# Kernel tuning notes

Measured on AMD Instinct MI355X. Metric: run time of the kernel, lower is better.

## Reference

```python
import jax, jax.numpy as jnp
import numpy as np

N, L, HID = 8192, 256, 128   # rows, input_len, hidden_size
H, NLIN = 2, 2               # n_heads, n_linear
EPS = 1e-5


def setup_inputs() -> dict:
    key = jax.random.key(0)
    ks = jax.random.split(key, 8)
    # attention params (torch.randn in source; scaled 0.02 for numerical sanity of softmax logits)
    Q = jax.random.normal(ks[0], (H, L, HID), jnp.float32) * 0.02
    K = jax.random.normal(ks[1], (H, L, HID), jnp.float32) * 0.02
    V_down = jax.random.normal(ks[2], (H, L, HID), jnp.float32) * 0.02
    V_up = jax.random.normal(ks[3], (H, HID, L), jnp.float32) * 0.02
    # nn.Linear(input_len, input_len): uniform(-1/sqrt(L), 1/sqrt(L))
    bnd = 1.0 / np.sqrt(L)
    W = jax.random.uniform(ks[4], (NLIN, L, L), jnp.float32, -bnd, bnd)
    b = jax.random.uniform(ks[5], (NLIN, L), jnp.float32, -bnd, bnd)
    x = jax.random.normal(ks[6], (N, L), jnp.float32)
    return {"x": x, "Q": Q, "K": K, "V_down": V_down, "V_up": V_up, "W": W, "b": b}


def _batch_norm(z):
    # custom BatchNorm1d: per-feature normalization over the batch (row) dim, no affine
    m = jnp.mean(z, axis=0, keepdims=True)
    v = jnp.var(z, axis=0, keepdims=True)
    return (z - m) * jax.lax.rsqrt(v + EPS)


def reference(x, Q, K, V_down, V_up, W, b):
    h = _batch_norm(x)                              # [N, L]
    dE = jnp.zeros_like(h)
    for i in range(Q.shape[0]):                     # small fixed head count
        q = h @ Q[i]                                # [N, HID]
        k = h @ K[i]                                # [N, HID]
        A = jax.nn.softmax(q @ k.T, axis=1)         # [N, N]
        dE = dE + A @ (h @ V_down[i]) @ V_up[i]     # low-rank value path
    h = _batch_norm(h + dE)
    for j in range(W.shape[0]):                     # per-row Linear+ReLU loop == batched matmul
        h = jax.nn.relu(h @ W[j].T + b[j])
    return h
```

## Files before the change

### kernel.cpp

```cpp
#include <hip/hip_runtime.h>
#include <hip/hip_bf16.h>

constexpr int Nrows = 8192;
constexpr int L     = 256;
constexpr int D     = 128;
constexpr float EPS = 1e-5f;

typedef __bf16 bf16x8 __attribute__((ext_vector_type(8)));
typedef __bf16 bf16x4 __attribute__((ext_vector_type(4)));
typedef float  f32x4  __attribute__((ext_vector_type(4)));

#define MFMA16(a, b, c) __builtin_amdgcn_mfma_f32_16x16x32_bf16((a), (b), (c), 0, 0, 0)

__global__ void k_cvt_params(const float* __restrict__ Q, const float* __restrict__ K,
                             const float* __restrict__ Vd, const float* __restrict__ Vup,
                             const float* __restrict__ W,
                             __bf16* __restrict__ Bt, __bf16* __restrict__ VupT,
                             __bf16* __restrict__ Wb) {
    int i = blockIdx.x * 256 + threadIdx.x;
    if (i < 6 * 128 * 256) {
        int g = i >> 15; int r = i & 32767; int d = r >> 8; int l = r & 255;
        const float* src = (g % 3 == 0 ? Q : (g % 3 == 1 ? K : Vd)) + (g / 3) * (L * D);
        Bt[i] = (__bf16)src[l * D + d];
    } else if (i < 8 * 128 * 256) {
        int j = i - 6 * 128 * 256;
        int h = j >> 15; int r = j & 32767; int l = r >> 7; int d = r & 127;
        VupT[j] = (__bf16)Vup[h * (D * L) + d * L + l];
    } else {
        int j = i - 8 * 128 * 256;
        Wb[j] = (__bf16)W[j];
    }
}

__global__ void k_bn_stats(const float* __restrict__ x, float* __restrict__ sum,
                           float* __restrict__ sq) {
    int col = threadIdx.x;
    int r0 = blockIdx.x * 32;
    float s = 0.f, s2 = 0.f;
    for (int i = 0; i < 32; i++) {
        float v = x[(r0 + i) * L + col];
        s += v; s2 += v * v;
    }
    atomicAdd(&sum[col], s);
    atomicAdd(&sq[col], s2);
}

__global__ void k_bn_norm1(const float* __restrict__ x, const float* __restrict__ sum,
                           const float* __restrict__ sq, __bf16* __restrict__ hb,
                           float* __restrict__ hf) {
    int i = (blockIdx.x * 256 + threadIdx.x) * 4;
    int col = i & (L - 1);
    f32x4 v = *(const f32x4*)(x + i);
    bf16x4 o; f32x4 of;
#pragma unroll
    for (int j = 0; j < 4; j++) {
        float m   = sum[col + j] * (1.0f / Nrows);
        float var = sq[col + j] * (1.0f / Nrows) - m * m;
        float rs  = rsqrtf(var + EPS);
        float t = (v[j] - m) * rs;
        of[j] = t; o[j] = (__bf16)t;
    }
    *(bf16x4*)(hb + i) = o;
    *(f32x4*)(hf + i) = of;
}

__launch_bounds__(256)
__global__ void k_gemm_qkv(const __bf16* __restrict__ h, const __bf16* __restrict__ Bt,
                           __bf16* __restrict__ q0, __bf16* __restrict__ k0,
                           __bf16* __restrict__ q1, __bf16* __restrict__ k1,
                           __bf16* __restrict__ Vt) {
    int g = blockIdx.y;
    int m0 = blockIdx.x * 64;
    int w = threadIdx.x >> 6, lane = threadIdx.x & 63;
    int c = lane & 15, qd = lane >> 4;
    int mw = m0 + w * 16;
    const __bf16* B = Bt + g * (128 * 256);

    f32x4 acc[8] = {};
#pragma unroll
    for (int kc = 0; kc < 8; kc++) {
        bf16x8 a = *(const bf16x8*)(h + (mw + c) * L + kc * 32 + qd * 8);
#pragma unroll
        for (int nt = 0; nt < 8; nt++) {
            bf16x8 b = *(const bf16x8*)(B + (nt * 16 + c) * L + kc * 32 + qd * 8);
            acc[nt] = MFMA16(a, b, acc[nt]);
        }
    }
    if (g == 2 || g == 5) {
        __bf16* vt = Vt + (g / 3) * (128 * Nrows);
#pragma unroll
        for (int nt = 0; nt < 8; nt++)
#pragma unroll
            for (int r = 0; r < 4; r++) {
                int row = mw + 4 * qd + r;
                int colv = nt * 16 + c;
                vt[colv * Nrows + row] = (__bf16)acc[nt][r];
            }
    } else {
        __bf16* dst = (g == 0) ? q0 : (g == 1) ? k0 : (g == 3) ? q1 : k1;
#pragma unroll
        for (int nt = 0; nt < 8; nt++)
#pragma unroll
            for (int r = 0; r < 4; r++) {
                int row = mw + 4 * qd + r;
                int colv = nt * 16 + c;
                dst[row * D + colv] = (__bf16)acc[nt][r];
            }
    }
}

__launch_bounds__(256, 1)
__global__ void k_flash(const __bf16* __restrict__ q0, const __bf16* __restrict__ k0,
                        const __bf16* __restrict__ q1, const __bf16* __restrict__ k1,
                        const __bf16* __restrict__ Vt, __bf16* __restrict__ O) {
    int head = blockIdx.x & 1;
    int qtile = blockIdx.x >> 1;
    int m0 = qtile * 64;
    const __bf16* qm = head ? q1 : q0;
    const __bf16* km = head ? k1 : k0;
    const __bf16* vt = Vt + head * (128 * Nrows);
    __bf16* Og = O + head * (Nrows * D);

    int w = threadIdx.x >> 6, lane = threadIdx.x & 63;
    int c = lane & 15, qd = lane >> 4;

    __shared__ __bf16 Pb[4][64 * 56];
    __shared__ float l_red[4][64];
    __shared__ float l_inv[64];
    __shared__ float obuf[4][64][16];

    bf16x8 aq[4][4];
#pragma unroll
    for (int mt = 0; mt < 4; mt++)
#pragma unroll
        for (int kc = 0; kc < 4; kc++)
            aq[mt][kc] = *(const bf16x8*)(qm + (m0 + mt * 16 + c) * D + kc * 32 + qd * 8);

    f32x4 oacc[4][8] = {};
    float lp[4][4] = {};
    __bf16* Pw = &Pb[w][0];

    auto loadkv = [&](bf16x8 (&kb)[2][4], bf16x8 (&vb)[8], int n0) {
        int nb = n0 + w * 32;
#pragma unroll
        for (int nt = 0; nt < 2; nt++)
#pragma unroll
            for (int kc = 0; kc < 4; kc++)
                kb[nt][kc] = *(const bf16x8*)(km + (nb + nt * 16 + c) * D + kc * 32 + qd * 8);
#pragma unroll
        for (int dvt = 0; dvt < 8; dvt++)
            vb[dvt] = *(const bf16x8*)(vt + (dvt * 16 + c) * Nrows + nb + qd * 8);
    };

    auto compute = [&](const bf16x8 (&kb)[2][4], const bf16x8 (&vb)[8]) {
#pragma unroll
        for (int nt = 0; nt < 2; nt++) {
            f32x4 s[4] = {};
            __builtin_amdgcn_s_setprio(1);
#pragma unroll
            for (int kc = 0; kc < 4; kc++) {
#pragma unroll
                for (int mt = 0; mt < 4; mt++) s[mt] = MFMA16(aq[mt][kc], kb[nt][kc], s[mt]);
            }
            __builtin_amdgcn_s_setprio(0);
#pragma unroll
            for (int mt = 0; mt < 4; mt++)
#pragma unroll
                for (int r = 0; r < 4; r++) {
                    float e = __expf(s[mt][r]);
                    lp[mt][r] += e;
                    Pw[(mt * 16 + 4 * qd + r) * 56 + nt * 16 + c] = (__bf16)e;
                }
        }
        bf16x8 ap[4];
#pragma unroll
        for (int mt = 0; mt < 4; mt++)
            ap[mt] = *(const bf16x8*)(Pw + (mt * 16 + c) * 56 + qd * 8);
        __builtin_amdgcn_s_setprio(1);
#pragma unroll
        for (int dvt = 0; dvt < 8; dvt++) {
#pragma unroll
            for (int mt = 0; mt < 4; mt++) oacc[mt][dvt] = MFMA16(ap[mt], vb[dvt], oacc[mt][dvt]);
        }
        __builtin_amdgcn_s_setprio(0);
    };

    bf16x8 kbA[2][4], vbA[8], kbB[2][4], vbB[8];
    loadkv(kbA, vbA, 0);
    for (int n0 = 0; n0 < Nrows; n0 += 256) {
        loadkv(kbB, vbB, n0 + 128);
        compute(kbA, vbA);
        if (n0 + 256 < Nrows)
            loadkv(kbA, vbA, n0 + 256);
        compute(kbB, vbB);
    }

#pragma unroll
    for (int mt = 0; mt < 4; mt++)
#pragma unroll
        for (int r = 0; r < 4; r++) {
            float v = lp[mt][r];
            v += __shfl_xor(v, 1, 16);
            v += __shfl_xor(v, 2, 16);
            v += __shfl_xor(v, 4, 16);
            v += __shfl_xor(v, 8, 16);
            lp[mt][r] = v;
        }
    if (c == 0) {
#pragma unroll
        for (int mt = 0; mt < 4; mt++)
#pragma unroll
            for (int r = 0; r < 4; r++)
                l_red[w][mt * 16 + 4 * qd + r] = lp[mt][r];
    }
    __syncthreads();
    if (threadIdx.x < 64)
        l_inv[threadIdx.x] = 1.0f / (l_red[0][threadIdx.x] + l_red[1][threadIdx.x] +
                                     l_red[2][threadIdx.x] + l_red[3][threadIdx.x]);

    for (int dvt = 0; dvt < 8; dvt++) {
        __syncthreads();
#pragma unroll
        for (int mt = 0; mt < 4; mt++)
#pragma unroll
            for (int r = 0; r < 4; r++)
                obuf[w][mt * 16 + 4 * qd + r][c] = oacc[mt][dvt][r];
        __syncthreads();
        int t = threadIdx.x;
        int row = (t * 4) >> 4, col = (t * 4) & 15;
        f32x4 v = *(const f32x4*)&obuf[0][row][col];
        f32x4 v1 = *(const f32x4*)&obuf[1][row][col];
        f32x4 v2 = *(const f32x4*)&obuf[2][row][col];
        f32x4 v3 = *(const f32x4*)&obuf[3][row][col];
        float il = l_inv[row];
        bf16x4 o;
#pragma unroll
        for (int e = 0; e < 4; e++) o[e] = (__bf16)((v[e] + v1[e] + v2[e] + v3[e]) * il);
        *(bf16x4*)(Og + (m0 + row) * D + dvt * 16 + col) = o;
    }
}

__launch_bounds__(256)
__global__ void k_gemm_vup(const __bf16* __restrict__ O, const __bf16* __restrict__ VupT,
                           const float* __restrict__ hf, float* __restrict__ z) {
    int n0 = blockIdx.y * 128;
    int m0 = blockIdx.x * 64;
    int w = threadIdx.x >> 6, lane = threadIdx.x & 63;
    int c = lane & 15, qd = lane >> 4;
    int mw = m0 + w * 16;

    f32x4 acc[8] = {};
#pragma unroll
    for (int kc = 0; kc < 8; kc++) {
        const __bf16* Oh = O + (kc >> 2) * (Nrows * D);
        const __bf16* Vh = VupT + (kc >> 2) * (L * D);
        int ko = (kc & 3) * 32 + qd * 8;
        bf16x8 a = *(const bf16x8*)(Oh + (mw + c) * D + ko);
#pragma unroll
        for (int nt = 0; nt < 8; nt++) {
            bf16x8 b = *(const bf16x8*)(Vh + (n0 + nt * 16 + c) * D + ko);
            acc[nt] = MFMA16(a, b, acc[nt]);
        }
    }
#pragma unroll
    for (int nt = 0; nt < 8; nt++)
#pragma unroll
        for (int r = 0; r < 4; r++) {
            int row = mw + 4 * qd + r;
            int col = n0 + nt * 16 + c;
            z[row * L + col] = acc[nt][r] + hf[row * L + col];
        }
}

__launch_bounds__(256)
__global__ void k_gemm_w_norm(const float* __restrict__ z, const float* __restrict__ sum,
                              const float* __restrict__ sq, const __bf16* __restrict__ W,
                              const float* __restrict__ bias, __bf16* __restrict__ out) {
    int n0 = blockIdx.y * 128;
    int m0 = blockIdx.x * 64;
    int w = threadIdx.x >> 6, lane = threadIdx.x & 63;
    int c = lane & 15, qd = lane >> 4;
    int mw = m0 + w * 16;

    f32x4 acc[8] = {};
#pragma unroll
    for (int kc = 0; kc < 8; kc++) {
        int k0 = kc * 32 + qd * 8;
        f32x4 s0 = *(const f32x4*)(sum + k0);
        f32x4 s1 = *(const f32x4*)(sum + k0 + 4);
        f32x4 v0 = *(const f32x4*)(sq + k0);
        f32x4 v1 = *(const f32x4*)(sq + k0 + 4);
        f32x4 za = *(const f32x4*)(z + (mw + c) * L + k0);
        f32x4 zb = *(const f32x4*)(z + (mw + c) * L + k0 + 4);
        bf16x8 a;
#pragma unroll
        for (int j = 0; j < 4; j++) {
            float m  = s0[j] * (1.0f / Nrows);
            float rs = rsqrtf(v0[j] * (1.0f / Nrows) - m * m + EPS);
            a[j] = (__bf16)((za[j] - m) * rs);
        }
#pragma unroll
        for (int j = 0; j < 4; j++) {
            float m  = s1[j] * (1.0f / Nrows);
            float rs = rsqrtf(v1[j] * (1.0f / Nrows) - m * m + EPS);
            a[4 + j] = (__bf16)((zb[j] - m) * rs);
        }
#pragma unroll
        for (int nt = 0; nt < 8; nt++) {
            bf16x8 b = *(const bf16x8*)(W + (n0 + nt * 16 + c) * L + kc * 32 + qd * 8);
            acc[nt] = MFMA16(a, b, acc[nt]);
        }
    }
#pragma unroll
    for (int nt = 0; nt < 8; nt++) {
        int col = n0 + nt * 16 + c;
        float bv = bias[col];
#pragma unroll
        for (int r = 0; r < 4; r++) {
            int row = mw + 4 * qd + r;
            float v = fmaxf(acc[nt][r] + bv, 0.0f);
            out[row * L + col] = (__bf16)v;
        }
    }
}

__launch_bounds__(256)
__global__ void k_gemm_w(const __bf16* __restrict__ hin, const __bf16* __restrict__ W,
                         const float* __restrict__ bias, float* __restrict__ out) {
    int n0 = blockIdx.y * 128;
    int m0 = blockIdx.x * 64;
    int w = threadIdx.x >> 6, lane = threadIdx.x & 63;
    int c = lane & 15, qd = lane >> 4;
    int mw = m0 + w * 16;

    f32x4 acc[8] = {};
#pragma unroll
    for (int kc = 0; kc < 8; kc++) {
        bf16x8 a = *(const bf16x8*)(hin + (mw + c) * L + kc * 32 + qd * 8);
#pragma unroll
        for (int nt = 0; nt < 8; nt++) {
            bf16x8 b = *(const bf16x8*)(W + (n0 + nt * 16 + c) * L + kc * 32 + qd * 8);
            acc[nt] = MFMA16(a, b, acc[nt]);
        }
    }
#pragma unroll
    for (int nt = 0; nt < 8; nt++) {
        int col = n0 + nt * 16 + c;
        float bv = bias[col];
#pragma unroll
        for (int r = 0; r < 4; r++) {
            int row = mw + 4 * qd + r;
            float v = fmaxf(acc[nt][r] + bv, 0.0f);
            out[row * L + col] = v;
        }
    }
}

extern "C" void kernel_launch(void* const* d_in, const int* in_sizes, int n_in,
                              void* d_out, int out_size, void* d_ws, size_t ws_size,
                              hipStream_t stream) {
    (void)in_sizes; (void)n_in; (void)out_size; (void)ws_size;
    const float* x   = (const float*)d_in[0];
    const float* Q   = (const float*)d_in[1];
    const float* K   = (const float*)d_in[2];
    const float* Vd  = (const float*)d_in[3];
    const float* Vup = (const float*)d_in[4];
    const float* W   = (const float*)d_in[5];
    const float* b   = (const float*)d_in[6];
    float* out = (float*)d_out;

    char* ws = (char*)d_ws;
    size_t off = 0;
    auto alloc = [&](size_t bytes) -> void* {
        void* p = ws + off;
        off += (bytes + 255) & ~(size_t)255;
        return p;
    };
    float*  stats = (float*)alloc(4 * 256 * sizeof(float));
    __bf16* Bt    = (__bf16*)alloc(6 * 128 * 256 * 2);
    __bf16* VupT  = (__bf16*)alloc(2 * 256 * 128 * 2);
    __bf16* Wb    = (__bf16*)alloc(2 * 256 * 256 * 2);
    __bf16* hb    = (__bf16*)alloc((size_t)Nrows * L * 2);
    float*  hf    = (float*)alloc((size_t)Nrows * L * 4);
    __bf16* q0    = (__bf16*)alloc((size_t)Nrows * D * 2);
    __bf16* k0    = (__bf16*)alloc((size_t)Nrows * D * 2);
    __bf16* q1    = (__bf16*)alloc((size_t)Nrows * D * 2);
    __bf16* k1    = (__bf16*)alloc((size_t)Nrows * D * 2);
    __bf16* Vt    = (__bf16*)alloc((size_t)2 * 128 * Nrows * 2);
    __bf16* O     = (__bf16*)alloc((size_t)2 * Nrows * D * 2);
    float*  z     = (float*)alloc((size_t)Nrows * L * 4);
    __bf16* h3    = (__bf16*)alloc((size_t)Nrows * L * 2);

    float* sum1 = stats, *sq1 = stats + 256, *sum2 = stats + 512, *sq2 = stats + 768;

    hipMemsetAsync(stats, 0, 4 * 256 * sizeof(float), stream);
    k_cvt_params<<<1536, 256, 0, stream>>>(Q, K, Vd, Vup, W, Bt, VupT, Wb);
    k_bn_stats<<<256, 256, 0, stream>>>(x, sum1, sq1);
    k_bn_norm1<<<2048, 256, 0, stream>>>(x, sum1, sq1, hb, hf);
    k_gemm_qkv<<<dim3(128, 6), 256, 0, stream>>>(hb, Bt, q0, k0, q1, k1, Vt);
    k_flash<<<256, 256, 0, stream>>>(q0, k0, q1, k1, Vt, O);
    k_gemm_vup<<<dim3(128, 2), 256, 0, stream>>>(O, VupT, hf, z);
    k_bn_stats<<<256, 256, 0, stream>>>(z, sum2, sq2);
    k_gemm_w_norm<<<dim3(128, 2), 256, 0, stream>>>(z, sum2, sq2, Wb, b, h3);
    k_gemm_w<<<dim3(128, 2), 256, 0, stream>>>(h3, Wb + 256 * 256, b + 256, out);
}
```

Measured before the change: 280.1 us.

## Halve flash query tile to 512 blocks and fuse BN stats into vup GEMM

```diff
diff --git a/kernel.cpp b/kernel.cpp
--- a/kernel.cpp
+++ b/kernel.cpp
@@ -109,13 +109,13 @@
     }
 }
 
-__launch_bounds__(256, 1)
+__launch_bounds__(256, 2)
 __global__ void k_flash(const __bf16* __restrict__ q0, const __bf16* __restrict__ k0,
                         const __bf16* __restrict__ q1, const __bf16* __restrict__ k1,
                         const __bf16* __restrict__ Vt, __bf16* __restrict__ O) {
     int head = blockIdx.x & 1;
     int qtile = blockIdx.x >> 1;
-    int m0 = qtile * 64;
+    int m0 = qtile * 32;
     const __bf16* qm = head ? q1 : q0;
     const __bf16* km = head ? k1 : k0;
     const __bf16* vt = Vt + head * (128 * Nrows);
@@ -124,47 +124,49 @@
     int w = threadIdx.x >> 6, lane = threadIdx.x & 63;
     int c = lane & 15, qd = lane >> 4;
 
-    __shared__ __bf16 Pb[4][64 * 56];
-    __shared__ float l_red[4][64];
-    __shared__ float l_inv[64];
-    __shared__ float obuf[4][64][16];
-
-    bf16x8 aq[4][4];
-#pragma unroll
-    for (int mt = 0; mt < 4; mt++)
+    __shared__ __bf16 Pb[4][32 * 56];
+    __shared__ float l_red[4][32];
+    __shared__ float l_inv[32];
+    __shared__ float obuf[4][32][16];
+
+    bf16x8 aq[2][4];
+#pragma unroll
+    for (int mt = 0; mt < 2; mt++)
 #pragma unroll
         for (int kc = 0; kc < 4; kc++)
             aq[mt][kc] = *(const bf16x8*)(qm + (m0 + mt * 16 + c) * D + kc * 32 + qd * 8);
 
-    f32x4 oacc[4][8] = {};
-    float lp[4][4] = {};
+    f32x4 oacc[2][8] = {};
+    float lp[2][4] = {};
     __bf16* Pw = &Pb[w][0];
 
-    auto loadkv = [&](bf16x8 (&kb)[2][4], bf16x8 (&vb)[8], int n0) {
+    auto loadk = [&](bf16x8 (&kb)[2][4], int n0) {
         int nb = n0 + w * 32;
 #pragma unroll
         for (int nt = 0; nt < 2; nt++)
 #pragma unroll
             for (int kc = 0; kc < 4; kc++)
                 kb[nt][kc] = *(const bf16x8*)(km + (nb + nt * 16 + c) * D + kc * 32 + qd * 8);
+    };
+    auto loadv = [&](bf16x8 (&vb)[8], int n0) {
+        int nb = n0 + w * 32;
 #pragma unroll
         for (int dvt = 0; dvt < 8; dvt++)
             vb[dvt] = *(const bf16x8*)(vt + (dvt * 16 + c) * Nrows + nb + qd * 8);
     };
-
     auto compute = [&](const bf16x8 (&kb)[2][4], const bf16x8 (&vb)[8]) {
 #pragma unroll
         for (int nt = 0; nt < 2; nt++) {
-            f32x4 s[4] = {};
+            f32x4 s[2] = {};
             __builtin_amdgcn_s_setprio(1);
 #pragma unroll
             for (int kc = 0; kc < 4; kc++) {
 #pragma unroll
-                for (int mt = 0; mt < 4; mt++) s[mt] = MFMA16(aq[mt][kc], kb[nt][kc], s[mt]);
+                for (int mt = 0; mt < 2; mt++) s[mt] = MFMA16(aq[mt][kc], kb[nt][kc], s[mt]);
             }
             __builtin_amdgcn_s_setprio(0);
 #pragma unroll
-            for (int mt = 0; mt < 4; mt++)
+            for (int mt = 0; mt < 2; mt++)
 #pragma unroll
                 for (int r = 0; r < 4; r++) {
                     float e = __expf(s[mt][r]);
@@ -172,31 +174,32 @@
                     Pw[(mt * 16 + 4 * qd + r) * 56 + nt * 16 + c] = (__bf16)e;
                 }
         }
-        bf16x8 ap[4];
-#pragma unroll
-        for (int mt = 0; mt < 4; mt++)
+        bf16x8 ap[2];
+#pragma unroll
+        for (int mt = 0; mt < 2; mt++)
             ap[mt] = *(const bf16x8*)(Pw + (mt * 16 + c) * 56 + qd * 8);
         __builtin_amdgcn_s_setprio(1);
 #pragma unroll
         for (int dvt = 0; dvt < 8; dvt++) {
 #pragma unroll
-            for (int mt = 0; mt < 4; mt++) oacc[mt][dvt] = MFMA16(ap[mt], vb[dvt], oacc[mt][dvt]);
+            for (int mt = 0; mt < 2; mt++) oacc[mt][dvt] = MFMA16(ap[mt], vb[dvt], oacc[mt][dvt]);
         }
         __builtin_amdgcn_s_setprio(0);
     };
 
-    bf16x8 kbA[2][4], vbA[8], kbB[2][4], vbB[8];
-    loadkv(kbA, vbA, 0);
+    bf16x8 kbA[2][4], kbB[2][4], vb[8];
+    loadk(kbA, 0);
     for (int n0 = 0; n0 < Nrows; n0 += 256) {
-        loadkv(kbB, vbB, n0 + 128);
-        compute(kbA, vbA);
-        if (n0 + 256 < Nrows)
-            loadkv(kbA, vbA, n0 + 256);
-        compute(kbB, vbB);
-    }
-
-#pragma unroll
-    for (int mt = 0; mt < 4; mt++)
+        loadk(kbB, n0 + 128);
+        loadv(vb, n0);
+        compute(kbA, vb);
+        if (n0 + 256 < Nrows) loadk(kbA, n0 + 256);
+        loadv(vb, n0 + 128);
+        compute(kbB, vb);
+    }
+
+#pragma unroll
+    for (int mt = 0; mt < 2; mt++)
 #pragma unroll
         for (int r = 0; r < 4; r++) {
             float v = lp[mt][r];
@@ -208,41 +211,45 @@
         }
     if (c == 0) {
 #pragma unroll
-        for (int mt = 0; mt < 4; mt++)
+        for (int mt = 0; mt < 2; mt++)
 #pragma unroll
             for (int r = 0; r < 4; r++)
                 l_red[w][mt * 16 + 4 * qd + r] = lp[mt][r];
     }
     __syncthreads();
-    if (threadIdx.x < 64)
+    if (threadIdx.x < 32)
         l_inv[threadIdx.x] = 1.0f / (l_red[0][threadIdx.x] + l_red[1][threadIdx.x] +
                                      l_red[2][threadIdx.x] + l_red[3][threadIdx.x]);
 
     for (int dvt = 0; dvt < 8; dvt++) {
         __syncthreads();
 #pragma unroll
-        for (int mt = 0; mt < 4; mt++)
+        for (int mt = 0; mt < 2; mt++)
 #pragma unroll
             for (int r = 0; r < 4; r++)
                 obuf[w][mt * 16 + 4 * qd + r][c] = oacc[mt][dvt][r];
         __syncthreads();
         int t = threadIdx.x;
-        int row = (t * 4) >> 4, col = (t * 4) & 15;
-        f32x4 v = *(const f32x4*)&obuf[0][row][col];
-        f32x4 v1 = *(const f32x4*)&obuf[1][row][col];
-        f32x4 v2 = *(const f32x4*)&obuf[2][row][col];
-        f32x4 v3 = *(const f32x4*)&obuf[3][row][col];
-        float il = l_inv[row];
-        bf16x4 o;
-#pragma unroll
-        for (int e = 0; e < 4; e++) o[e] = (__bf16)((v[e] + v1[e] + v2[e] + v3[e]) * il);
-        *(bf16x4*)(Og + (m0 + row) * D + dvt * 16 + col) = o;
+        if (t < 128) {
+            int row = t >> 2;
+            int col = (t & 3) * 4;
+            f32x4 v = *(const f32x4*)&obuf[0][row][col];
+            f32x4 v1 = *(const f32x4*)&obuf[1][row][col];
+            f32x4 v2 = *(const f32x4*)&obuf[2][row][col];
+            f32x4 v3 = *(const f32x4*)&obuf[3][row][col];
+            float il = l_inv[row];
+            bf16x4 o;
+#pragma unroll
+            for (int e = 0; e < 4; e++) o[e] = (__bf16)((v[e] + v1[e] + v2[e] + v3[e]) * il);
+            *(bf16x4*)(Og + (m0 + row) * D + dvt * 16 + col) = o;
+        }
     }
 }
 
 __launch_bounds__(256)
 __global__ void k_gemm_vup(const __bf16* __restrict__ O, const __bf16* __restrict__ VupT,
-                           const float* __restrict__ hf, float* __restrict__ z) {
+                           const float* __restrict__ hf, float* __restrict__ z,
+                           float* __restrict__ sum2, float* __restrict__ sq2) {
     int n0 = blockIdx.y * 128;
     int m0 = blockIdx.x * 64;
     int w = threadIdx.x >> 6, lane = threadIdx.x & 63;
@@ -263,13 +270,23 @@
         }
     }
 #pragma unroll
-    for (int nt = 0; nt < 8; nt++)
+    for (int nt = 0; nt < 8; nt++) {
+        int col = n0 + nt * 16 + c;
+        float s = 0.f, s2 = 0.f;
 #pragma unroll
         for (int r = 0; r < 4; r++) {
             int row = mw + 4 * qd + r;
-            int col = n0 + nt * 16 + c;
-            z[row * L + col] = acc[nt][r] + hf[row * L + col];
-        }
+            float zv = acc[nt][r] + hf[row * L + col];
+            z[row * L + col] = zv;
+            s += zv; s2 += zv * zv;
+        }
+        s  += __shfl_xor(s, 16);  s  += __shfl_xor(s, 32);
+        s2 += __shfl_xor(s2, 16); s2 += __shfl_xor(s2, 32);
+        if (qd == 0) {
+            atomicAdd(&sum2[col], s);
+            atomicAdd(&sq2[col], s2);
+        }
+    }
 }
 
 __launch_bounds__(256)
@@ -398,9 +415,8 @@
     k_bn_stats<<<256, 256, 0, stream>>>(x, sum1, sq1);
     k_bn_norm1<<<2048, 256, 0, stream>>>(x, sum1, sq1, hb, hf);
     k_gemm_qkv<<<dim3(128, 6), 256, 0, stream>>>(hb, Bt, q0, k0, q1, k1, Vt);
-    k_flash<<<256, 256, 0, stream>>>(q0, k0, q1, k1, Vt, O);
-    k_gemm_vup<<<dim3(128, 2), 256, 0, stream>>>(O, VupT, hf, z);
-    k_bn_stats<<<256, 256, 0, stream>>>(z, sum2, sq2);
+    k_flash<<<512, 256, 0, stream>>>(q0, k0, q1, k1, Vt, O);
+    k_gemm_vup<<<dim3(128, 2), 256, 0, stream>>>(O, VupT, hf, z, sum2, sq2);
     k_gemm_w_norm<<<dim3(128, 2), 256, 0, stream>>>(z, sum2, sq2, Wb, b, h3);
     k_gemm_w<<<dim3(128, 2), 256, 0, stream>>>(h3, Wb + 256 * 256, b + 256, out);
 }
```

Result: slower. 398.2 us (+42.2%).
